# Performance work log

Hardware: AMD Instinct MI355X
Metric: run time of the kernel (lower is better)

## Reference

```python
import jax, jax.numpy as jnp
import numpy as np

B, S, D, H = 4, 1024, 1024, 16
DH = D // H  # head dim = 64
PAD = -1e7   # padding_num in source
EPS = 1e-3   # keras LayerNormalization default epsilon


def setup_inputs() -> dict:
    key = jax.random.key(0)
    ks = jax.random.split(key, 8)
    return {
        "queries": jax.random.normal(ks[0], (B, S, D), jnp.float32),
        "keys": jax.random.normal(ks[1], (B, S, D), jnp.float32),
        "values": jax.random.normal(ks[2], (B, S, D), jnp.float32),
        "query_masks": jax.random.randint(ks[3], (B, S), 0, 2, jnp.int32),
        "key_masks": jax.random.randint(ks[4], (B, S), 0, 2, jnp.int32),
        "Wq": jax.random.normal(ks[5], (D, D), jnp.float32) * (D ** -0.5),
        "Wk": jax.random.normal(ks[6], (D, D), jnp.float32) * (D ** -0.5),
        "Wv": jax.random.normal(ks[7], (D, D), jnp.float32) * (D ** -0.5),
        "gamma": jnp.ones((D,), jnp.float32),
        "beta": jnp.zeros((D,), jnp.float32),
    }


def reference(queries, keys, values, query_masks, key_masks, Wq, Wk, Wv, gamma, beta):
    # QKV projections (no bias)
    Q = queries @ Wq  # [B,S,D]
    K = keys @ Wk
    V = values @ Wv
    # split heads: tf.split(axis=2)+concat(axis=0) == head-major layout [H,B,S,DH]
    Qh = Q.reshape(B, S, H, DH).transpose(2, 0, 1, 3)
    Kh = K.reshape(B, S, H, DH).transpose(2, 0, 1, 3)
    Vh = V.reshape(B, S, H, DH).transpose(2, 0, 1, 3)
    # scaled scores; note source scales by head_dim ** 0.5 (d_k of split K)
    scores = jnp.einsum("hbqd,hbkd->hbqk", Qh, Kh) / (DH ** 0.5)
    # additive key mask: positions where key_mask==0 get large negative
    scores = jnp.where(key_masks[None, :, None, :] == 0, PAD, scores)
    attn = jax.nn.softmax(scores, axis=-1)
    # multiplicative query mask AFTER softmax (as in source)
    attn = attn * query_masks[None, :, :, None].astype(jnp.float32)
    out = jnp.einsum("hbqk,hbkd->hbqd", attn, Vh)  # [H,B,S,DH]
    # merge heads back: concat over feature axis in head order
    out = out.transpose(1, 2, 0, 3).reshape(B, S, D)
    # residual + LayerNorm
    res = queries + out
    mean = jnp.mean(res, axis=-1, keepdims=True)
    var = jnp.mean(jnp.square(res - mean), axis=-1, keepdims=True)
    return gamma * (res - mean) * jax.lax.rsqrt(var + EPS) + beta
```

## Files before the change

### kernel.cpp

```cpp
#include <hip/hip_runtime.h>

#define BB   4
#define SS   1024
#define DD   1024
#define HH   16
#define DHH  64
#define LN_EPS  (1e-3f)

typedef unsigned short u16;
typedef __attribute__((ext_vector_type(8))) short bf16x8;
typedef __attribute__((ext_vector_type(4))) float f32x4;

__device__ __forceinline__ u16 f2bf(float f) {
    union { float f; unsigned int u; } v; v.f = f;
    return (u16)((v.u + 0x7FFFu + ((v.u >> 16) & 1u)) >> 16);
}

__device__ __forceinline__ void cp16(void* lds, const void* g) {
    __builtin_amdgcn_global_load_lds(
        (const __attribute__((address_space(1))) unsigned int*)g,
        (__attribute__((address_space(3))) unsigned int*)lds, 16, 0, 0);
}

__global__ __launch_bounds__(256) void prep(const float* __restrict__ q,
                                            const float* __restrict__ k,
                                            const float* __restrict__ v,
                                            const float* __restrict__ Wq,
                                            const float* __restrict__ Wk,
                                            const float* __restrict__ Wv,
                                            u16* __restrict__ Abf,
                                            u16* __restrict__ WtA) {
    __shared__ float Ts[64][65];
    const int z = blockIdx.z;
    const int tid = threadIdx.x;
    if (z < 3) {
        const float* src = (z == 0) ? q : (z == 1) ? k : v;
        u16* dst = Abf + (size_t)z * ((size_t)BB * SS * DD);
        const int N8 = BB * SS * DD / 8;
        for (int i = blockIdx.x * 256 + tid; i < N8; i += 256 * 256) {
            const float4 f0 = ((const float4*)src)[i * 2];
            const float4 f1 = ((const float4*)src)[i * 2 + 1];
            union { u16 u[8]; uint4 o; } t;
            t.u[0] = f2bf(f0.x); t.u[1] = f2bf(f0.y);
            t.u[2] = f2bf(f0.z); t.u[3] = f2bf(f0.w);
            t.u[4] = f2bf(f1.x); t.u[5] = f2bf(f1.y);
            t.u[6] = f2bf(f1.z); t.u[7] = f2bf(f1.w);
            ((uint4*)dst)[i] = t.o;
        }
    } else {
        const float* W = (z == 3) ? Wq : (z == 4) ? Wk : Wv;
        u16* Wt = WtA + (size_t)(z - 3) * DD * DD;
        const int k0 = (blockIdx.x >> 4) * 64, n0 = (blockIdx.x & 15) * 64;
        #pragma unroll
        for (int it = 0; it < 4; ++it) {
            const int idx = tid + it * 256;
            const int r = idx >> 4, c4 = (idx & 15) * 4;
            const float4 vv = *(const float4*)&W[(size_t)(k0 + r) * DD + n0 + c4];
            Ts[r][c4 + 0] = vv.x; Ts[r][c4 + 1] = vv.y;
            Ts[r][c4 + 2] = vv.z; Ts[r][c4 + 3] = vv.w;
        }
        __syncthreads();
        const int n = tid >> 2, kc = (tid & 3) * 16;
        #pragma unroll
        for (int p = 0; p < 8; ++p) {
            const unsigned int lo = f2bf(Ts[kc + p * 2 + 0][n]);
            const unsigned int hi = f2bf(Ts[kc + p * 2 + 1][n]);
            *(unsigned int*)&Wt[(size_t)(n0 + n) * DD + k0 + kc + p * 2] = lo | (hi << 16);
        }
    }
}

__global__ __launch_bounds__(256) void gemm_fused(const u16* __restrict__ Abf,
                                                  const u16* __restrict__ WtA,
                                                  u16* __restrict__ Qbf,
                                                  u16* __restrict__ Kbf,
                                                  u16* __restrict__ Vtb) {
    __shared__ u16 As[128 * 64];
    __shared__ u16 Bs[128 * 64];
    const int bid = blockIdx.x;
    const int xcd = bid & 7;
    const int t   = bid >> 3;
    const int z   = t >> 5;
    const int rr  = t & 31;
    const int m0  = (xcd * 4 + (rr & 3)) * 128;
    const int n0  = (rr >> 2) * 128;

    const u16* A = Abf + (size_t)z * BB * SS * DD;
    const u16* B = WtA + (size_t)z * DD * DD;
    const int tid  = threadIdx.x;
    const int wave = tid >> 6, lane = tid & 63;
    const int ln = lane & 15, quad = lane >> 4;
    const int mw = (wave & 1) * 64, nw = (wave >> 1) * 64;

    f32x4 acc[4][4] = {};

    for (int k0 = 0; k0 < DD; k0 += 64) {
        __syncthreads();
        #pragma unroll
        for (int w = 0; w < 4; ++w) {
            const int s = w * 256 + wave * 64 + lane;
            const int r = s >> 3, csrc = (s & 7) ^ (r & 7);
            cp16(&As[(size_t)(w * 256 + wave * 64) * 8],
                 &A[(size_t)(m0 + r) * DD + k0 + csrc * 8]);
            cp16(&Bs[(size_t)(w * 256 + wave * 64) * 8],
                 &B[(size_t)(n0 + r) * DD + k0 + csrc * 8]);
        }
        __syncthreads();

        #pragma unroll
        for (int kk = 0; kk < 2; ++kk) {
            bf16x8 af[4], bfv[4];
            #pragma unroll
            for (int i = 0; i < 4; ++i) {
                const int r = mw + i * 16 + ln;
                af[i] = *(const bf16x8*)&As[((r << 3) + ((kk * 4 + quad) ^ (r & 7))) << 3];
            }
            #pragma unroll
            for (int j = 0; j < 4; ++j) {
                const int r = nw + j * 16 + ln;
                bfv[j] = *(const bf16x8*)&Bs[((r << 3) + ((kk * 4 + quad) ^ (r & 7))) << 3];
            }
            #pragma unroll
            for (int i = 0; i < 4; ++i)
                #pragma unroll
                for (int j = 0; j < 4; ++j)
                    acc[i][j] = __builtin_amdgcn_mfma_f32_16x16x32_bf16(af[i], bfv[j], acc[i][j], 0, 0, 0);
        }
    }

    if (z < 2) {
        u16* C = (z == 0) ? Qbf : Kbf;
        const float scale = (z == 0) ? 0.125f : 1.0f;
        #pragma unroll
        for (int i = 0; i < 4; ++i) {
            const int mbase = m0 + mw + i * 16 + quad * 4;
            const int bb = mbase >> 10, sb = mbase & 1023;
            #pragma unroll
            for (int j = 0; j < 4; ++j) {
                const int n = n0 + nw + j * 16 + ln;
                const int hh = n >> 6, dh = n & 63;
                #pragma unroll
                for (int r = 0; r < 4; ++r)
                    C[(((size_t)bb * HH + hh) * SS + sb + r) * DHH + dh] =
                        f2bf(acc[i][j][r] * scale);
            }
        }
    } else {
        #pragma unroll
        for (int i = 0; i < 4; ++i) {
            const int mbase = m0 + mw + i * 16 + quad * 4;
            const int bb = mbase >> 10, sb = mbase & 1023;
            #pragma unroll
            for (int j = 0; j < 4; ++j) {
                const int n = n0 + nw + j * 16 + ln;
                const int hh = n >> 6, dh = n & 63;
                uint2 pk;
                pk.x = (unsigned int)f2bf(acc[i][j][0]) | ((unsigned int)f2bf(acc[i][j][1]) << 16);
                pk.y = (unsigned int)f2bf(acc[i][j][2]) | ((unsigned int)f2bf(acc[i][j][3]) << 16);
                *(uint2*)&Vtb[(((size_t)bb * HH + hh) * DHH + dh) * SS + sb] = pk;
            }
        }
    }
}

__global__ __launch_bounds__(256) void attn_mfma(const u16* __restrict__ Qg,
                                                 const u16* __restrict__ Kg,
                                                 const u16* __restrict__ Vtg,
                                                 const int* __restrict__ qmask,
                                                 const int* __restrict__ kmask,
                                                 float* __restrict__ O) {
    __shared__ u16 QPs[64 * 68];
    __shared__ u16 Ks[64 * 64];
    __shared__ u16 Vs[64 * 64];

    const int bid  = blockIdx.x;
    const int xcd  = bid & 7;
    const int rest = bid >> 3;
    const int bh   = (rest & 7) * 8 + xcd;
    const int qt   = rest >> 3;
    const int b    = bh >> 4, h = bh & 15;
    const int q0   = qt * 64;
    const int tid  = threadIdx.x;
    const int wave = tid >> 6, lane = tid & 63;
    const int ln = lane & 15, quad = lane >> 4;
    const size_t bhs = (size_t)b * HH + h;

    #pragma unroll
    for (int w = 0; w < 2; ++w) {
        const int s = w * 256 + wave * 64 + lane;
        const int r = s >> 3, csrc = (s & 7) ^ (r & 7);
        cp16(&QPs[(size_t)(w * 256 + wave * 64) * 8],
             &Qg[(bhs * SS + q0 + r) * DHH + csrc * 8]);
    }
    __syncthreads();

    bf16x8 qf[2];
    #pragma unroll
    for (int kk = 0; kk < 2; ++kk) {
        const int r = wave * 16 + ln;
        qf[kk] = *(const bf16x8*)&QPs[((r << 3) + ((kk * 4 + quad) ^ (r & 7))) << 3];
    }

    f32x4 o[4] = {};
    float lsum[4] = {0.f, 0.f, 0.f, 0.f};
    const f32x4 zero = {0.f, 0.f, 0.f, 0.f};

    for (int kt = 0; kt < SS / 64; ++kt) {
        __syncthreads();
        #pragma unroll
        for (int w = 0; w < 2; ++w) {
            const int s = w * 256 + wave * 64 + lane;
            const int r = s >> 3, csrc = (s & 7) ^ (r & 7);
            cp16(&Ks[(size_t)(w * 256 + wave * 64) * 8],
                 &Kg[(bhs * SS + kt * 64 + r) * DHH + csrc * 8]);
            cp16(&Vs[(size_t)(w * 256 + wave * 64) * 8],
                 &Vtg[(bhs * DHH + r) * SS + kt * 64 + csrc * 8]);
        }
        __syncthreads();

        #pragma unroll
        for (int nt = 0; nt < 4; ++nt) {
            const int krow = nt * 16 + ln;
            const bf16x8 k0f = *(const bf16x8*)&Ks[((krow << 3) + ((0 + quad) ^ (krow & 7))) << 3];
            const bf16x8 k1f = *(const bf16x8*)&Ks[((krow << 3) + ((4 + quad) ^ (krow & 7))) << 3];
            f32x4 sacc = __builtin_amdgcn_mfma_f32_16x16x32_bf16(qf[0], k0f, zero, 0, 0, 0);
            sacc = __builtin_amdgcn_mfma_f32_16x16x32_bf16(qf[1], k1f, sacc, 0, 0, 0);
            const int km = kmask[b * SS + kt * 64 + krow];
            #pragma unroll
            for (int r = 0; r < 4; ++r) {
                const float p = km ? __expf(sacc[r]) : 0.0f;
                lsum[r] += p;
                QPs[(wave * 16 + quad * 4 + r) * 68 + nt * 16 + ln] = f2bf(p);
            }
        }

        #pragma unroll
        for (int kk2 = 0; kk2 < 2; ++kk2) {
            const bf16x8 pf = *(const bf16x8*)&QPs[(wave * 16 + ln) * 68 + kk2 * 32 + quad * 8];
            #pragma unroll
            for (int nt2 = 0; nt2 < 4; ++nt2) {
                const int vrow = nt2 * 16 + ln;
                const bf16x8 vf = *(const bf16x8*)&Vs[((vrow << 3) + ((kk2 * 4 + quad) ^ (vrow & 7))) << 3];
                o[nt2] = __builtin_amdgcn_mfma_f32_16x16x32_bf16(pf, vf, o[nt2], 0, 0, 0);
            }
        }
    }

    #pragma unroll
    for (int r = 0; r < 4; ++r) {
        #pragma unroll
        for (int off = 1; off < 16; off <<= 1)
            lsum[r] += __shfl_xor(lsum[r], off);
        const int q = q0 + wave * 16 + quad * 4 + r;
        const float scale = (float)qmask[b * SS + q] / lsum[r];
        #pragma unroll
        for (int nt2 = 0; nt2 < 4; ++nt2)
            O[((size_t)b * SS + q) * DD + h * DHH + nt2 * 16 + ln] = o[nt2][r] * scale;
    }
}

__global__ __launch_bounds__(256) void ln_kernel(const float* __restrict__ Qin,
                                                 const float* __restrict__ attn,
                                                 const float* __restrict__ gamma,
                                                 const float* __restrict__ beta,
                                                 float* __restrict__ out) {
    const int row = blockIdx.x;
    const int tid = threadIdx.x;
    const int wid = tid >> 6, lane = tid & 63;
    __shared__ float sred[4];

    const float4 qv = ((const float4*)Qin)[(size_t)row * 256 + tid];
    const float4 av = ((const float4*)attn)[(size_t)row * 256 + tid];
    float4 v;
    v.x = qv.x + av.x; v.y = qv.y + av.y;
    v.z = qv.z + av.z; v.w = qv.w + av.w;

    float sum = v.x + v.y + v.z + v.w;
    #pragma unroll
    for (int off = 32; off; off >>= 1) sum += __shfl_down(sum, off);
    if (lane == 0) sred[wid] = sum;
    __syncthreads();
    const float mean = (sred[0] + sred[1] + sred[2] + sred[3]) * (1.0f / DD);
    __syncthreads();

    const float dx = v.x - mean, dy = v.y - mean, dz = v.z - mean, dw = v.w - mean;
    float vs = dx * dx + dy * dy + dz * dz + dw * dw;
    #pragma unroll
    for (int off = 32; off; off >>= 1) vs += __shfl_down(vs, off);
    if (lane == 0) sred[wid] = vs;
    __syncthreads();
    const float var = (sred[0] + sred[1] + sred[2] + sred[3]) * (1.0f / DD);
    const float inv = rsqrtf(var + LN_EPS);

    const float4 g = ((const float4*)gamma)[tid];
    const float4 bt = ((const float4*)beta)[tid];
    float4 ov;
    ov.x = g.x * dx * inv + bt.x; ov.y = g.y * dy * inv + bt.y;
    ov.z = g.z * dz * inv + bt.z; ov.w = g.w * dw * inv + bt.w;
    ((float4*)out)[(size_t)row * 256 + tid] = ov;
}

extern "C" void kernel_launch(void* const* d_in, const int* in_sizes, int n_in,
                              void* d_out, int out_size, void* d_ws, size_t ws_size,
                              hipStream_t stream) {
    const float* queries = (const float*)d_in[0];
    const float* keys    = (const float*)d_in[1];
    const float* values  = (const float*)d_in[2];
    const int*   qmask   = (const int*)d_in[3];
    const int*   kmask   = (const int*)d_in[4];
    const float* Wq      = (const float*)d_in[5];
    const float* Wk      = (const float*)d_in[6];
    const float* Wv      = (const float*)d_in[7];
    const float* gamma   = (const float*)d_in[8];
    const float* beta    = (const float*)d_in[9];
    float* out = (float*)d_out;

    const size_t NTOK = (size_t)BB * SS;
    u16* Abf = (u16*)d_ws;
    float* Ob = (float*)d_ws;
    u16* Qbf = Abf + 3 * NTOK * DD;
    u16* Kbf = Qbf + NTOK * DD;
    u16* Vtb = Kbf + NTOK * DD;
    u16* WtA = Vtb + NTOK * DD;

    prep<<<dim3(256, 1, 6), 256, 0, stream>>>(queries, keys, values, Wq, Wk, Wv, Abf, WtA);

    gemm_fused<<<768, 256, 0, stream>>>(Abf, WtA, Qbf, Kbf, Vtb);

    attn_mfma<<<BB * HH * (SS / 64), 256, 0, stream>>>(Qbf, Kbf, Vtb, qmask, kmask, Ob);

    ln_kernel<<<BB * SS, 256, 0, stream>>>(queries, Ob, gamma, beta, out);
}
```

Before: 204.9 us.

## Fuse all stages into one cooperative persistent kernel with grid syncs

Merges the prep, QKV GEMM, attention and LayerNorm kernels into a single cooperative persistent kernel, with grid-wide syncs between phases and a fallback to four separate launches. It also splits the V projection into 128x64 tiles so the GEMM phase has 1024 work items instead of 768, which balances it across the persistent grid. The aim is to remove inter-kernel launch gaps and tail effects. In exchange it adds grid-sync overhead, occupancy queries on every call, and shared-memory sizing fixed by the largest phase, which may limit occupancy.

```diff
diff --git a/kernel.cpp b/kernel.cpp
--- a/kernel.cpp
+++ b/kernel.cpp
@@ -1,4 +1,7 @@
 #include <hip/hip_runtime.h>
+#include <hip/hip_cooperative_groups.h>
+
+namespace cg = cooperative_groups;
 
 #define BB   4
 #define SS   1024
@@ -6,6 +9,7 @@
 #define HH   16
 #define DHH  64
 #define LN_EPS  (1e-3f)
+#define NTT  ((size_t)BB * SS * DD)
 
 typedef unsigned short u16;
 typedef __attribute__((ext_vector_type(8))) short bf16x8;
@@ -22,77 +26,77 @@
         (__attribute__((address_space(3))) unsigned int*)lds, 16, 0, 0);
 }
 
-__global__ __launch_bounds__(256) void prep(const float* __restrict__ q,
-                                            const float* __restrict__ k,
-                                            const float* __restrict__ v,
+
+__device__ __forceinline__ void phase_conv(const float* __restrict__ q,
+                                           const float* __restrict__ k,
+                                           const float* __restrict__ v,
+                                           u16* __restrict__ Abf,
+                                           int gtid, int nthr) {
+    const int total = (int)(3 * NTT / 8);
+    for (int i = gtid; i < total; i += nthr) {
+        const float* s = (i < 524288) ? q : (i < 1048576) ? k : v;
+        const int off = i & 524287;
+        const float4 f0 = ((const float4*)s)[off * 2];
+        const float4 f1 = ((const float4*)s)[off * 2 + 1];
+        union { u16 u[8]; uint4 o; } t;
+        t.u[0] = f2bf(f0.x); t.u[1] = f2bf(f0.y);
+        t.u[2] = f2bf(f0.z); t.u[3] = f2bf(f0.w);
+        t.u[4] = f2bf(f1.x); t.u[5] = f2bf(f1.y);
+        t.u[6] = f2bf(f1.z); t.u[7] = f2bf(f1.w);
+        ((uint4*)Abf)[i] = t.o;
+    }
+}
+
+__device__ __forceinline__ void phase_wtile(u16* __restrict__ smem, int vb,
                                             const float* __restrict__ Wq,
                                             const float* __restrict__ Wk,
                                             const float* __restrict__ Wv,
-                                            u16* __restrict__ Abf,
                                             u16* __restrict__ WtA) {
-    __shared__ float Ts[64][65];
-    const int z = blockIdx.z;
+    float (*Ts)[65] = (float (*)[65])smem;
     const int tid = threadIdx.x;
-    if (z < 3) {
-        const float* src = (z == 0) ? q : (z == 1) ? k : v;
-        u16* dst = Abf + (size_t)z * ((size_t)BB * SS * DD);
-        const int N8 = BB * SS * DD / 8;
-        for (int i = blockIdx.x * 256 + tid; i < N8; i += 256 * 256) {
-            const float4 f0 = ((const float4*)src)[i * 2];
-            const float4 f1 = ((const float4*)src)[i * 2 + 1];
-            union { u16 u[8]; uint4 o; } t;
-            t.u[0] = f2bf(f0.x); t.u[1] = f2bf(f0.y);
-            t.u[2] = f2bf(f0.z); t.u[3] = f2bf(f0.w);
-            t.u[4] = f2bf(f1.x); t.u[5] = f2bf(f1.y);
-            t.u[6] = f2bf(f1.z); t.u[7] = f2bf(f1.w);
-            ((uint4*)dst)[i] = t.o;
-        }
-    } else {
-        const float* W = (z == 3) ? Wq : (z == 4) ? Wk : Wv;
-        u16* Wt = WtA + (size_t)(z - 3) * DD * DD;
-        const int k0 = (blockIdx.x >> 4) * 64, n0 = (blockIdx.x & 15) * 64;
-        #pragma unroll
-        for (int it = 0; it < 4; ++it) {
-            const int idx = tid + it * 256;
-            const int r = idx >> 4, c4 = (idx & 15) * 4;
-            const float4 vv = *(const float4*)&W[(size_t)(k0 + r) * DD + n0 + c4];
-            Ts[r][c4 + 0] = vv.x; Ts[r][c4 + 1] = vv.y;
-            Ts[r][c4 + 2] = vv.z; Ts[r][c4 + 3] = vv.w;
-        }
-        __syncthreads();
-        const int n = tid >> 2, kc = (tid & 3) * 16;
-        #pragma unroll
-        for (int p = 0; p < 8; ++p) {
-            const unsigned int lo = f2bf(Ts[kc + p * 2 + 0][n]);
-            const unsigned int hi = f2bf(Ts[kc + p * 2 + 1][n]);
-            *(unsigned int*)&Wt[(size_t)(n0 + n) * DD + k0 + kc + p * 2] = lo | (hi << 16);
-        }
-    }
-}
-
-__global__ __launch_bounds__(256) void gemm_fused(const u16* __restrict__ Abf,
-                                                  const u16* __restrict__ WtA,
-                                                  u16* __restrict__ Qbf,
-                                                  u16* __restrict__ Kbf,
-                                                  u16* __restrict__ Vtb) {
-    __shared__ u16 As[128 * 64];
-    __shared__ u16 Bs[128 * 64];
-    const int bid = blockIdx.x;
-    const int xcd = bid & 7;
-    const int t   = bid >> 3;
-    const int z   = t >> 5;
-    const int rr  = t & 31;
-    const int m0  = (xcd * 4 + (rr & 3)) * 128;
-    const int n0  = (rr >> 2) * 128;
-
-    const u16* A = Abf + (size_t)z * BB * SS * DD;
-    const u16* B = WtA + (size_t)z * DD * DD;
+    const float* W = (vb < 256) ? Wq : (vb < 512) ? Wk : Wv;
+    u16* Wt = WtA + (size_t)(vb >> 8) * DD * DD;
+    const int idx = vb & 255;
+    const int k0 = (idx >> 4) * 64, n0 = (idx & 15) * 64;
+    __syncthreads();
+    #pragma unroll
+    for (int it = 0; it < 4; ++it) {
+        const int i2 = tid + it * 256;
+        const int r = i2 >> 4, c4 = (i2 & 15) * 4;
+        const float4 vv = *(const float4*)&W[(size_t)(k0 + r) * DD + n0 + c4];
+        Ts[r][c4 + 0] = vv.x; Ts[r][c4 + 1] = vv.y;
+        Ts[r][c4 + 2] = vv.z; Ts[r][c4 + 3] = vv.w;
+    }
+    __syncthreads();
+    const int n = tid >> 2, kc = (tid & 3) * 16;
+    #pragma unroll
+    for (int p = 0; p < 8; ++p) {
+        const unsigned int lo = f2bf(Ts[kc + p * 2 + 0][n]);
+        const unsigned int hi = f2bf(Ts[kc + p * 2 + 1][n]);
+        *(unsigned int*)&Wt[(size_t)(n0 + n) * DD + k0 + kc + p * 2] = lo | (hi << 16);
+    }
+}
+
+template <int NJ>
+__device__ __forceinline__ void gemm_tile(u16* __restrict__ smem,
+                                          const u16* __restrict__ A,
+                                          const u16* __restrict__ B,
+                                          int m0, int n0, int z,
+                                          u16* __restrict__ Qbf,
+                                          u16* __restrict__ Kbf,
+                                          u16* __restrict__ Vtb) {
+    u16* As = smem;
+    u16* Bs = smem + 8192;
     const int tid  = threadIdx.x;
     const int wave = tid >> 6, lane = tid & 63;
     const int ln = lane & 15, quad = lane >> 4;
-    const int mw = (wave & 1) * 64, nw = (wave >> 1) * 64;
-
-    f32x4 acc[4][4] = {};
+    const int mw = (wave & 1) * 64, nw = (wave >> 1) * (NJ * 16);
+
+    f32x4 acc[4][NJ];
+    #pragma unroll
+    for (int i = 0; i < 4; ++i)
+        #pragma unroll
+        for (int j = 0; j < NJ; ++j) acc[i][j] = (f32x4){0.f, 0.f, 0.f, 0.f};
 
     for (int k0 = 0; k0 < DD; k0 += 64) {
         __syncthreads();
@@ -102,6 +106,11 @@
             const int r = s >> 3, csrc = (s & 7) ^ (r & 7);
             cp16(&As[(size_t)(w * 256 + wave * 64) * 8],
                  &A[(size_t)(m0 + r) * DD + k0 + csrc * 8]);
+        }
+        #pragma unroll
+        for (int w = 0; w < NJ; ++w) {
+            const int s = w * 256 + wave * 64 + lane;
+            const int r = s >> 3, csrc = (s & 7) ^ (r & 7);
             cp16(&Bs[(size_t)(w * 256 + wave * 64) * 8],
                  &B[(size_t)(n0 + r) * DD + k0 + csrc * 8]);
         }
@@ -109,21 +118,21 @@
 
         #pragma unroll
         for (int kk = 0; kk < 2; ++kk) {
-            bf16x8 af[4], bfv[4];
+            bf16x8 af[4], bfv[NJ];
             #pragma unroll
             for (int i = 0; i < 4; ++i) {
                 const int r = mw + i * 16 + ln;
                 af[i] = *(const bf16x8*)&As[((r << 3) + ((kk * 4 + quad) ^ (r & 7))) << 3];
             }
             #pragma unroll
-            for (int j = 0; j < 4; ++j) {
+            for (int j = 0; j < NJ; ++j) {
                 const int r = nw + j * 16 + ln;
                 bfv[j] = *(const bf16x8*)&Bs[((r << 3) + ((kk * 4 + quad) ^ (r & 7))) << 3];
             }
             #pragma unroll
             for (int i = 0; i < 4; ++i)
                 #pragma unroll
-                for (int j = 0; j < 4; ++j)
+                for (int j = 0; j < NJ; ++j)
                     acc[i][j] = __builtin_amdgcn_mfma_f32_16x16x32_bf16(af[i], bfv[j], acc[i][j], 0, 0, 0);
         }
     }
@@ -136,7 +145,7 @@
             const int mbase = m0 + mw + i * 16 + quad * 4;
             const int bb = mbase >> 10, sb = mbase & 1023;
             #pragma unroll
-            for (int j = 0; j < 4; ++j) {
+            for (int j = 0; j < NJ; ++j) {
                 const int n = n0 + nw + j * 16 + ln;
                 const int hh = n >> 6, dh = n & 63;
                 #pragma unroll
@@ -151,7 +160,7 @@
             const int mbase = m0 + mw + i * 16 + quad * 4;
             const int bb = mbase >> 10, sb = mbase & 1023;
             #pragma unroll
-            for (int j = 0; j < 4; ++j) {
+            for (int j = 0; j < NJ; ++j) {
                 const int n = n0 + nw + j * 16 + ln;
                 const int hh = n >> 6, dh = n & 63;
                 uint2 pk;
@@ -163,34 +172,55 @@
     }
 }
 
-__global__ __launch_bounds__(256) void attn_mfma(const u16* __restrict__ Qg,
-                                                 const u16* __restrict__ Kg,
-                                                 const u16* __restrict__ Vtg,
-                                                 const int* __restrict__ qmask,
-                                                 const int* __restrict__ kmask,
-                                                 float* __restrict__ O) {
-    __shared__ u16 QPs[64 * 68];
-    __shared__ u16 Ks[64 * 64];
-    __shared__ u16 Vs[64 * 64];
-
-    const int bid  = blockIdx.x;
-    const int xcd  = bid & 7;
-    const int rest = bid >> 3;
+__device__ __forceinline__ void phase_gemm(u16* __restrict__ smem, int vb,
+                                           const u16* __restrict__ Abf,
+                                           const u16* __restrict__ WtA,
+                                           u16* __restrict__ Qbf,
+                                           u16* __restrict__ Kbf,
+                                           u16* __restrict__ Vtb) {
+    const int z = (vb < 256) ? 0 : (vb < 512) ? 1 : 2;
+    const int xcd = vb & 7;
+    const u16* A = Abf + (size_t)z * NTT;
+    const u16* B = WtA + (size_t)z * DD * DD;
+    if (z < 2) {
+        const int t = (vb & 255) >> 3;
+        gemm_tile<4>(smem, A, B, (xcd * 4 + (t & 3)) * 128, (t >> 2) * 128,
+                     z, Qbf, Kbf, Vtb);
+    } else {
+        const int t = (vb - 512) >> 3;
+        gemm_tile<2>(smem, A, B, (xcd * 4 + (t & 3)) * 128, (t >> 2) * 64,
+                     z, Qbf, Kbf, Vtb);
+    }
+}
+
+__device__ __forceinline__ void phase_attn(u16* __restrict__ smem, int vb,
+                                           const u16* __restrict__ Qbf,
+                                           const u16* __restrict__ Kbf,
+                                           const u16* __restrict__ Vtb,
+                                           const int* __restrict__ qmask,
+                                           const int* __restrict__ kmask,
+                                           float* __restrict__ Ob) {
+    u16* QPs = smem;
+    u16* Ks  = smem + 4352;
+    u16* Vs  = smem + 8448;
+    const int tid  = threadIdx.x;
+    const int wave = tid >> 6, lane = tid & 63;
+    const int ln = lane & 15, quad = lane >> 4;
+    const int xcd  = vb & 7;
+    const int rest = vb >> 3;
     const int bh   = (rest & 7) * 8 + xcd;
     const int qt   = rest >> 3;
     const int b    = bh >> 4, h = bh & 15;
     const int q0   = qt * 64;
-    const int tid  = threadIdx.x;
-    const int wave = tid >> 6, lane = tid & 63;
-    const int ln = lane & 15, quad = lane >> 4;
     const size_t bhs = (size_t)b * HH + h;
 
+    __syncthreads();
     #pragma unroll
     for (int w = 0; w < 2; ++w) {
         const int s = w * 256 + wave * 64 + lane;
         const int r = s >> 3, csrc = (s & 7) ^ (r & 7);
         cp16(&QPs[(size_t)(w * 256 + wave * 64) * 8],
-             &Qg[(bhs * SS + q0 + r) * DHH + csrc * 8]);
+             &Qbf[(bhs * SS + q0 + r) * DHH + csrc * 8]);
     }
     __syncthreads();
 
@@ -212,9 +242,9 @@
             const int s = w * 256 + wave * 64 + lane;
             const int r = s >> 3, csrc = (s & 7) ^ (r & 7);
             cp16(&Ks[(size_t)(w * 256 + wave * 64) * 8],
-                 &Kg[(bhs * SS + kt * 64 + r) * DHH + csrc * 8]);
+                 &Kbf[(bhs * SS + kt * 64 + r) * DHH + csrc * 8]);
             cp16(&Vs[(size_t)(w * 256 + wave * 64) * 8],
-                 &Vtg[(bhs * DHH + r) * SS + kt * 64 + csrc * 8]);
+                 &Vtb[(bhs * DHH + r) * SS + kt * 64 + csrc * 8]);
         }
         __syncthreads();
 
@@ -251,31 +281,29 @@
         #pragma unroll
         for (int off = 1; off < 16; off <<= 1)
             lsum[r] += __shfl_xor(lsum[r], off);
-        const int q = q0 + wave * 16 + quad * 4 + r;
-        const float scale = (float)qmask[b * SS + q] / lsum[r];
+        const int qq = q0 + wave * 16 + quad * 4 + r;
+        const float scale = (float)qmask[b * SS + qq] / lsum[r];
         #pragma unroll
         for (int nt2 = 0; nt2 < 4; ++nt2)
-            O[((size_t)b * SS + q) * DD + h * DHH + nt2 * 16 + ln] = o[nt2][r] * scale;
-    }
-}
-
-__global__ __launch_bounds__(256) void ln_kernel(const float* __restrict__ Qin,
-                                                 const float* __restrict__ attn,
-                                                 const float* __restrict__ gamma,
-                                                 const float* __restrict__ beta,
-                                                 float* __restrict__ out) {
-    const int row = blockIdx.x;
+            Ob[((size_t)b * SS + qq) * DD + h * DHH + nt2 * 16 + ln] = o[nt2][r] * scale;
+    }
+}
+
+__device__ __forceinline__ void phase_ln(int row, float* __restrict__ sred,
+                                         const float* __restrict__ q,
+                                         const float* __restrict__ Ob,
+                                         const float* __restrict__ gamma,
+                                         const float* __restrict__ beta,
+                                         float* __restrict__ out) {
     const int tid = threadIdx.x;
     const int wid = tid >> 6, lane = tid & 63;
-    __shared__ float sred[4];
-
-    const float4 qv = ((const float4*)Qin)[(size_t)row * 256 + tid];
-    const float4 av = ((const float4*)attn)[(size_t)row * 256 + tid];
-    float4 v;
-    v.x = qv.x + av.x; v.y = qv.y + av.y;
-    v.z = qv.z + av.z; v.w = qv.w + av.w;
-
-    float sum = v.x + v.y + v.z + v.w;
+    const float4 qv = ((const float4*)q)[(size_t)row * 256 + tid];
+    const float4 av = ((const float4*)Ob)[(size_t)row * 256 + tid];
+    float4 vv;
+    vv.x = qv.x + av.x; vv.y = qv.y + av.y;
+    vv.z = qv.z + av.z; vv.w = qv.w + av.w;
+
+    float sum = vv.x + vv.y + vv.z + vv.w;
     #pragma unroll
     for (int off = 32; off; off >>= 1) sum += __shfl_down(sum, off);
     if (lane == 0) sred[wid] = sum;
@@ -283,7 +311,8 @@
     const float mean = (sred[0] + sred[1] + sred[2] + sred[3]) * (1.0f / DD);
     __syncthreads();
 
-    const float dx = v.x - mean, dy = v.y - mean, dz = v.z - mean, dw = v.w - mean;
+    const float dx = vv.x - mean, dy = vv.y - mean;
+    const float dz = vv.z - mean, dw = vv.w - mean;
     float vs = dx * dx + dy * dy + dz * dz + dw * dw;
     #pragma unroll
     for (int off = 32; off; off >>= 1) vs += __shfl_down(vs, off);
@@ -292,12 +321,88 @@
     const float var = (sred[0] + sred[1] + sred[2] + sred[3]) * (1.0f / DD);
     const float inv = rsqrtf(var + LN_EPS);
 
-    const float4 g = ((const float4*)gamma)[tid];
+    const float4 g  = ((const float4*)gamma)[tid];
     const float4 bt = ((const float4*)beta)[tid];
     float4 ov;
     ov.x = g.x * dx * inv + bt.x; ov.y = g.y * dy * inv + bt.y;
     ov.z = g.z * dz * inv + bt.z; ov.w = g.w * dw * inv + bt.w;
     ((float4*)out)[(size_t)row * 256 + tid] = ov;
+    __syncthreads();
+}
+
+__global__ __launch_bounds__(256, 4) void fused_all(
+    const float* __restrict__ q, const float* __restrict__ k,
+    const float* __restrict__ v, const int* __restrict__ qmask,
+    const int* __restrict__ kmask, const float* __restrict__ Wq,
+    const float* __restrict__ Wk, const float* __restrict__ Wv,
+    const float* __restrict__ gamma, const float* __restrict__ beta,
+    float* __restrict__ out, u16* __restrict__ ws) {
+
+    __shared__ __align__(16) u16 smem[16384];
+    cg::grid_group grid = cg::this_grid();
+
+    const int bid = blockIdx.x, nb = gridDim.x;
+    const int tid = threadIdx.x;
+
+    u16*   Abf = ws;
+    float* Ob  = (float*)ws;
+    u16*   Qbf = ws + 3 * NTT;
+    u16*   Kbf = Qbf + NTT;
+    u16*   Vtb = Kbf + NTT;
+    u16*   WtA = Vtb + NTT;
+
+    for (int vb = bid; vb < 768; vb += nb)
+        phase_wtile(smem, vb, Wq, Wk, Wv, WtA);
+    phase_conv(q, k, v, Abf, bid * 256 + tid, nb * 256);
+
+    grid.sync();
+
+    for (int vb = bid; vb < 1024; vb += nb)
+        phase_gemm(smem, vb, Abf, WtA, Qbf, Kbf, Vtb);
+
+    grid.sync();
+
+    for (int vb = bid; vb < 1024; vb += nb)
+        phase_attn(smem, vb, Qbf, Kbf, Vtb, qmask, kmask, Ob);
+
+    grid.sync();
+
+    float* sred = (float*)smem;
+    for (int row = bid * 4; row < BB * SS; row += nb * 4)
+        #pragma unroll
+        for (int rr = 0; rr < 4; ++rr)
+            phase_ln(row + rr, sred, q, Ob, gamma, beta, out);
+}
+
+__global__ __launch_bounds__(256, 4) void k_prep(
+    const float* q, const float* k, const float* v,
+    const float* Wq, const float* Wk, const float* Wv,
+    u16* Abf, u16* WtA) {
+    __shared__ __align__(16) u16 smem[16384];
+    if (blockIdx.x < 768) phase_wtile(smem, blockIdx.x, Wq, Wk, Wv, WtA);
+    phase_conv(q, k, v, Abf, blockIdx.x * 256 + threadIdx.x, gridDim.x * 256);
+}
+
+__global__ __launch_bounds__(256, 4) void k_gemm(
+    const u16* Abf, const u16* WtA, u16* Qbf, u16* Kbf, u16* Vtb) {
+    __shared__ __align__(16) u16 smem[16384];
+    phase_gemm(smem, blockIdx.x, Abf, WtA, Qbf, Kbf, Vtb);
+}
+
+__global__ __launch_bounds__(256, 4) void k_attn(
+    const u16* Qbf, const u16* Kbf, const u16* Vtb,
+    const int* qmask, const int* kmask, float* Ob) {
+    __shared__ __align__(16) u16 smem[16384];
+    phase_attn(smem, blockIdx.x, Qbf, Kbf, Vtb, qmask, kmask, Ob);
+}
+
+__global__ __launch_bounds__(256) void k_ln(
+    const float* q, const float* Ob, const float* gamma, const float* beta,
+    float* out) {
+    __shared__ float sred[4];
+    #pragma unroll
+    for (int rr = 0; rr < 4; ++rr)
+        phase_ln(blockIdx.x * 4 + rr, sred, q, Ob, gamma, beta, out);
 }
 
 extern "C" void kernel_launch(void* const* d_in, const int* in_sizes, int n_in,
@@ -314,20 +419,44 @@
     const float* gamma   = (const float*)d_in[8];
     const float* beta    = (const float*)d_in[9];
     float* out = (float*)d_out;
-
-    const size_t NTOK = (size_t)BB * SS;
-    u16* Abf = (u16*)d_ws;
-    float* Ob = (float*)d_ws;
-    u16* Qbf = Abf + 3 * NTOK * DD;
-    u16* Kbf = Qbf + NTOK * DD;
-    u16* Vtb = Kbf + NTOK * DD;
-    u16* WtA = Vtb + NTOK * DD;
-
-    prep<<<dim3(256, 1, 6), 256, 0, stream>>>(queries, keys, values, Wq, Wk, Wv, Abf, WtA);
-
-    gemm_fused<<<768, 256, 0, stream>>>(Abf, WtA, Qbf, Kbf, Vtb);
-
-    attn_mfma<<<BB * HH * (SS / 64), 256, 0, stream>>>(Qbf, Kbf, Vtb, qmask, kmask, Ob);
-
-    ln_kernel<<<BB * SS, 256, 0, stream>>>(queries, Ob, gamma, beta, out);
-}
+    u16* ws = (u16*)d_ws;
+
+    int dev = 0;
+    (void)hipGetDevice(&dev);
+    int nCU = 0;
+    (void)hipDeviceGetAttribute(&nCU, hipDeviceAttributeMultiprocessorCount, dev);
+    int occ = 0;
+    (void)hipOccupancyMaxActiveBlocksPerMultiprocessor(&occ, fused_all, 256, 0);
+    long maxb = (long)occ * (long)nCU;
+
+    void* args[] = {
+        (void*)&queries, (void*)&keys, (void*)&values,
+        (void*)&qmask, (void*)&kmask,
+        (void*)&Wq, (void*)&Wk, (void*)&Wv,
+        (void*)&gamma, (void*)&beta,
+        (void*)&out, (void*)&ws
+    };
+
+    bool done = false;
+    long g = (maxb < 1024) ? maxb : 1024;
+    for (; g >= 256 && !done; g >>= 1) {
+        hipError_t e = hipLaunchCooperativeKernel((void*)fused_all,
+                                                  dim3((unsigned)g), dim3(256),
+                                                  args, 0, stream);
+        if (e == hipSuccess) done = true;
+        else (void)hipGetLastError();
+    }
+
+    if (!done) {
+        u16*   Abf = ws;
+        float* Ob  = (float*)ws;
+        u16*   Qbf = ws + 3 * NTT;
+        u16*   Kbf = Qbf + NTT;
+        u16*   Vtb = Kbf + NTT;
+        u16*   WtA = Vtb + NTT;
+        k_prep<<<1024, 256, 0, stream>>>(queries, keys, values, Wq, Wk, Wv, Abf, WtA);
+        k_gemm<<<1024, 256, 0, stream>>>(Abf, WtA, Qbf, Kbf, Vtb);
+        k_attn<<<1024, 256, 0, stream>>>(Qbf, Kbf, Vtb, qmask, kmask, Ob);
+        k_ln<<<1024, 256, 0, stream>>>(queries, Ob, gamma, beta, out);
+    }
+}
```

Result: slower. 430.3 us (+110.0%).
